# Kernel tuning notes

Measured on AMD Instinct MI355X. Metric: run time of the kernel, lower is better.

The kernel has to match this reference:

```python
import jax, jax.numpy as jnp
import numpy as np

B, NF, E, A = 4096, 40, 64, 32  # batch, num feature fields, embedding_size, attention_size


def setup_inputs() -> dict:
    key = jax.random.key(0)
    kx, kw, kb, kh = jax.random.split(key, 4)
    return {
        "x": jax.random.normal(kx, (B, NF, E), dtype=jnp.float32),
        "W": jax.random.normal(kw, (E, A), dtype=jnp.float32) * 0.05,  # random_normal init
        "b": jax.random.normal(kb, (A,), dtype=jnp.float32) * 0.05,
        "h": jax.random.normal(kh, (A,), dtype=jnp.float32) * 0.05,
        "p": jnp.ones((E, 1), dtype=jnp.float32),  # 'ones' initializer
    }


def reference(x, W, b, h, p):
    nf = x.shape[1]
    # pairwise (i<j) element-wise products, same ordering as the double loop
    ii, jj = np.triu_indices(nf, k=1)
    ewp = x[:, ii, :] * x[:, jj, :]                      # (B, P, E), P = nf*(nf-1)/2
    # attention MLP: relu(ewp @ W + b) . h, then exp-normalize over pairs
    a = jax.nn.relu(jnp.einsum('bpe,ea->bpa', ewp, W) + b)  # (B, P, A)
    e = jnp.exp(jnp.sum(a * h, axis=-1))                 # (B, P)  (faithful: no max-subtract)
    att = e / jnp.sum(e, axis=1, keepdims=True)          # (B, P)
    pooled = jnp.einsum('bp,bpe->be', att, ewp)          # attention-weighted sum over pairs
    return pooled @ p                                    # (B, 1)
```

## Files before the change

kernel.cpp:

```cpp
#include <hip/hip_runtime.h>

#define NFEAT 40
#define EMB   64
#define ATT   32
#define NPAIR 780
#define NTILE 49
#define XH_S  72
#define XREG  (NFEAT * XH_S)

#define WS_PRT   0
#define WS_WF    1024
#define WS_CONST 4096

typedef __attribute__((ext_vector_type(8))) _Float16 f16x8;
typedef __attribute__((ext_vector_type(4))) float    f32x4;
typedef __attribute__((ext_vector_type(2))) unsigned u32x2;

template <int CTRL>
__device__ __forceinline__ float dpp_add_f(float v) {
  int t = __builtin_amdgcn_update_dpp(0, __float_as_int(v), CTRL, 0xF, 0xF, true);
  return v + __int_as_float(t);
}
__device__ __forceinline__ float rowsum16(float v) {
  v = dpp_add_f<0x128>(v);
  v = dpp_add_f<0x124>(v);
  v = dpp_add_f<0x122>(v);
  v = dpp_add_f<0x121>(v);
  return v;
}
__device__ __forceinline__ float xgroup_sum(float v) {
#if __has_builtin(__builtin_amdgcn_permlane16_swap) && __has_builtin(__builtin_amdgcn_permlane32_swap)
  {
    auto a = __builtin_amdgcn_permlane16_swap(__float_as_uint(v), __float_as_uint(v), false, false);
    v = __uint_as_float(a[0]) + __uint_as_float(a[1]);
    auto b = __builtin_amdgcn_permlane32_swap(__float_as_uint(v), __float_as_uint(v), false, false);
    v = __uint_as_float(b[0]) + __uint_as_float(b[1]);
  }
#else
  v += __shfl_xor(v, 16, 64);
  v += __shfl_xor(v, 32, 64);
#endif
  return v;
}
__device__ __forceinline__ int pair_off(int i) { return 39 * i - (i * (i - 1)) / 2; }

extern "C" __global__ __launch_bounds__(256)
void afm_pre(const float* __restrict__ Wg, const float* __restrict__ bg,
             const float* __restrict__ hg, const float* __restrict__ pg,
             unsigned* __restrict__ ws) {
  __shared__ float Wl[EMB * ATT];
  const int tid = threadIdx.x;
  const float L2E = 1.4426950408889634f;

  if (blockIdx.x == 0) {
    for (int f = tid; f < EMB * ATT / 4; f += 256)
      *(float4*)&Wl[f * 4] = ((const float4*)Wg)[f];
    __syncthreads();
    for (int o = tid; o < 1536; o += 256) {
      int lane = o / 24, rem = o % 24, frag = rem >> 2, pi = rem & 3;
      int kk = frag / 3, which = frag % 3;
      int l15 = lane & 15, hk = lane >> 4;
      unsigned out = 0;
#pragma unroll
      for (int s = 0; s < 2; s++) {
        int t = pi * 2 + s;
        int krow = kk * 32 + hk * 8 + t;
        float v = (which == 0) ? Wl[krow * ATT + l15]
                : (which == 1) ? Wl[krow * ATT + 16 + l15]
                               : ((l15 == 0) ? pg[krow] : 0.f);
        _Float16 hv = (_Float16)v;
        unsigned short bits = __builtin_bit_cast(unsigned short, hv);
        out |= (unsigned)bits << (16 * s);
      }
      ws[WS_WF + lane * 24 + rem] = out;
    }
  } else if (blockIdx.x == 1) {
    for (int p = tid; p < NTILE * 16; p += 256) {
      int i = 0, j = 0;
      if (p < NPAIR) {
        i = (int)((79.0f - sqrtf(6241.0f - 8.0f * (float)p)) * 0.5f);
        if (i < 0) i = 0;
        while (pair_off(i + 1) <= p) ++i;
        while (pair_off(i) > p) --i;
        j = i + 1 + (p - pair_off(i));
      }
      int t = p >> 4, l = p & 15;
      ws[WS_PRT + (t >> 1) * 32 + l * 2 + (t & 1)] =
          (unsigned)(i * 144) | ((unsigned)(j * 144) << 16);
    }
  } else if (blockIdx.x == 2) {
    for (int o = tid; o < 1024; o += 256) {
      int lane = o >> 4, r = o & 15;
      int hk = lane >> 4, g = r >> 2, e = r & 3;
      float v;
      if (g == 0)      v = bg[hk * 4 + e];
      else if (g == 1) v = bg[16 + hk * 4 + e];
      else if (g == 2) v = hg[hk * 4 + e] * L2E;
      else             v = hg[16 + hk * 4 + e] * L2E;
      ((float*)ws)[WS_CONST + o] = v;
    }
  }
}

extern "C" __global__ __launch_bounds__(128)
void afm_kernel(const float* __restrict__ xg, const unsigned* __restrict__ ws,
                float* __restrict__ outg, int nbatch) {
  __shared__ __align__(16) _Float16 xh[2 * XREG];

  const int lane = threadIdx.x & 63, wid = threadIdx.x >> 6;
  const int l15 = lane & 15, hk = lane >> 4;
  const int bb = blockIdx.x * 2 + wid;
  if (bb >= nbatch) return;

  union { uint4 u; f16x8 h; } cv;
  const uint4* wfp = (const uint4*)(ws + WS_WF + lane * 24);
  f16x8 wf0[2], wf1[2], wf2[2];
  cv.u = wfp[0]; wf0[0] = cv.h;
  cv.u = wfp[1]; wf1[0] = cv.h;
  cv.u = wfp[2]; wf2[0] = cv.h;
  cv.u = wfp[3]; wf0[1] = cv.h;
  cv.u = wfp[4]; wf1[1] = cv.h;
  cv.u = wfp[5]; wf2[1] = cv.h;
  const float4* cp = (const float4*)((const float*)ws + WS_CONST + lane * 16);
  const float4 c0 = cp[0], c1 = cp[1];
  const float4 h0 = cp[2], h1 = cp[3];
  const f32x4 cb0 = {c0.x, c0.y, c0.z, c0.w};
  const f32x4 cb1 = {c1.x, c1.y, c1.z, c1.w};
  const f32x4 kz  = {0.f, 0.f, 0.f, 0.f};

  _Float16* xw = &xh[wid * XREG];
  const float* xsrc = xg + (size_t)bb * (NFEAT * EMB);
#pragma unroll
  for (int it = 0; it < 5; it++) {
    int g0 = (it * 64 + lane) * 8;
    float4 a = *(const float4*)&xsrc[g0];
    float4 b = *(const float4*)&xsrc[g0 + 4];
    int row = g0 >> 6, c = g0 & 63;
    f16x8 v = {(_Float16)a.x, (_Float16)a.y, (_Float16)a.z, (_Float16)a.w,
               (_Float16)b.x, (_Float16)b.y, (_Float16)b.z, (_Float16)b.w};
    *(f16x8*)&xw[row * XH_S + c] = v;
  }

  const unsigned wh = (unsigned)(wid * (XREG * 2) + hk * 16);
  float sum_e = 0.f, sum_es = 0.f;

  auto tile = [&](unsigned pij, bool full) {
    const unsigned offi = (pij & 0xFFFFu) + wh;
    const unsigned offj = (pij >> 16) + wh;
    const f16x8 xi0 = *(const f16x8*)((const char*)xh + offi);
    const f16x8 xj0 = *(const f16x8*)((const char*)xh + offj);
    const f16x8 xi1 = *(const f16x8*)((const char*)xh + offi + 64);
    const f16x8 xj1 = *(const f16x8*)((const char*)xh + offj + 64);
    f16x8 af0 = xi0 * xj0;
    f16x8 af1 = xi1 * xj1;
    f32x4 a0 = __builtin_amdgcn_mfma_f32_16x16x32_f16(wf0[0], af0, cb0, 0, 0, 0);
    f32x4 a1 = __builtin_amdgcn_mfma_f32_16x16x32_f16(wf1[0], af0, cb1, 0, 0, 0);
    f32x4 a2 = __builtin_amdgcn_mfma_f32_16x16x32_f16(wf2[0], af0, kz, 0, 0, 0);
    a0 = __builtin_amdgcn_mfma_f32_16x16x32_f16(wf0[1], af1, a0, 0, 0, 0);
    a1 = __builtin_amdgcn_mfma_f32_16x16x32_f16(wf1[1], af1, a1, 0, 0, 0);
    a2 = __builtin_amdgcn_mfma_f32_16x16x32_f16(wf2[1], af1, a2, 0, 0, 0);
    float t0 = fmaf(fmaxf(a0[0], 0.f), h0.x, fmaxf(a0[1], 0.f) * h0.y);
    float t1 = fmaf(fmaxf(a0[2], 0.f), h0.z, fmaxf(a0[3], 0.f) * h0.w);
    float t2 = fmaf(fmaxf(a1[0], 0.f), h1.x, fmaxf(a1[1], 0.f) * h1.y);
    float t3 = fmaf(fmaxf(a1[2], 0.f), h1.z, fmaxf(a1[3], 0.f) * h1.w);
    float v = xgroup_sum((t0 + t1) + (t2 + t3));
    float e = exp2f(v);
    if (!full) e = (l15 < 12) ? e : 0.f;
    sum_e += e;
    sum_es = fmaf(e, a2[0], sum_es);
  };

  u32x2 pp = *(const u32x2*)(ws + WS_PRT + l15 * 2);
#pragma unroll 4
  for (int k = 0; k < 24; ++k) {
    const unsigned pij0 = pp[0], pij1 = pp[1];
    if (k < 23) pp = *(const u32x2*)(ws + WS_PRT + (k + 1) * 32 + l15 * 2);
    tile(pij0, true);
    tile(pij1, true);
  }
  tile(ws[WS_PRT + 24 * 32 + l15 * 2], false);

  sum_e  = rowsum16(sum_e);
  sum_es = rowsum16(sum_es);
  if (lane == 0) outg[bb] = sum_es / sum_e;
}

extern "C" void kernel_launch(void* const* d_in, const int* in_sizes, int n_in,
                              void* d_out, int out_size, void* d_ws, size_t ws_size,
                              hipStream_t stream) {
  const float* xg = (const float*)d_in[0];
  const float* Wg = (const float*)d_in[1];
  const float* bg = (const float*)d_in[2];
  const float* hg = (const float*)d_in[3];
  const float* pg = (const float*)d_in[4];
  float* outg = (float*)d_out;
  unsigned* ws = (unsigned*)d_ws;
  const int Bn = in_sizes[0] / (NFEAT * EMB);
  afm_pre<<<dim3(3), dim3(256), 0, stream>>>(Wg, bg, hg, pg, ws);
  afm_kernel<<<dim3((Bn + 1) / 2), dim3(128), 0, stream>>>(xg, ws, outg, Bn);
}
```

Baseline: 41.38 us.

## Pack relu-dot epilogue into fp16 fdot2 and widen blocks to four waves

The attention epilogue now packs pairs of MFMA outputs to fp16, applies relu with a packed max and reduces against fp16-packed h using fdot2. This replaces eight scalar fmax/fma operations per tile. Blocks grow from two to four waves (one batch row each), the loop unroll rises to 8, and the x fp32→fp16 staging uses cvt_pkrtz. The change also adds a __syncthreads that is not needed, since each wave reads only its own shared-memory slice, and it lowers the precision of the h·relu dot.

New measurement: 41.61 us. No clear change (+0.6%).

```diff
diff --git a/kernel.cpp b/kernel.cpp
--- a/kernel.cpp
+++ b/kernel.cpp
@@ -15,6 +15,7 @@
 typedef __attribute__((ext_vector_type(8))) _Float16 f16x8;
 typedef __attribute__((ext_vector_type(4))) float    f32x4;
 typedef __attribute__((ext_vector_type(2))) unsigned u32x2;
+typedef __attribute__((ext_vector_type(2))) __fp16   h2_t;
 
 template <int CTRL>
 __device__ __forceinline__ float dpp_add_f(float v) {
@@ -43,6 +44,16 @@
   return v;
 }
 __device__ __forceinline__ int pair_off(int i) { return 39 * i - (i * (i - 1)) / 2; }
+
+__device__ __forceinline__ float reludot2(float s0, float s1, h2_t h2, float c) {
+  h2_t r = __builtin_amdgcn_cvt_pkrtz(s0, s1);
+  r = __builtin_elementwise_max(r, h2_t{(__fp16)0.f, (__fp16)0.f});
+#if __has_builtin(__builtin_amdgcn_fdot2)
+  return __builtin_amdgcn_fdot2(r, h2, c, false);
+#else
+  return fmaf((float)r[0], (float)h2[0], fmaf((float)r[1], (float)h2[1], c));
+#endif
+}
 
 extern "C" __global__ __launch_bounds__(256)
 void afm_pre(const float* __restrict__ Wg, const float* __restrict__ bg,
@@ -69,8 +80,7 @@
                 : (which == 1) ? Wl[krow * ATT + 16 + l15]
                                : ((l15 == 0) ? pg[krow] : 0.f);
         _Float16 hv = (_Float16)v;
-        unsigned short bits = __builtin_bit_cast(unsigned short, hv);
-        out |= (unsigned)bits << (16 * s);
+        out |= (unsigned)__builtin_bit_cast(unsigned short, hv) << (16 * s);
       }
       ws[WS_WF + lane * 24 + rem] = out;
     }
@@ -91,25 +101,31 @@
   } else if (blockIdx.x == 2) {
     for (int o = tid; o < 1024; o += 256) {
       int lane = o >> 4, r = o & 15;
-      int hk = lane >> 4, g = r >> 2, e = r & 3;
-      float v;
-      if (g == 0)      v = bg[hk * 4 + e];
-      else if (g == 1) v = bg[16 + hk * 4 + e];
-      else if (g == 2) v = hg[hk * 4 + e] * L2E;
-      else             v = hg[16 + hk * 4 + e] * L2E;
-      ((float*)ws)[WS_CONST + o] = v;
+      int hk = lane >> 4;
+      unsigned out;
+      if (r < 4) out = __float_as_uint(bg[hk * 4 + r]);
+      else if (r < 8) out = __float_as_uint(bg[16 + hk * 4 + (r - 4)]);
+      else if (r < 12) {
+        int q = r - 8;
+        int a0 = (q < 2) ? (hk * 4 + 2 * q) : (16 + hk * 4 + 2 * (q - 2));
+        __fp16 lo = (__fp16)(hg[a0] * L2E);
+        __fp16 hi = (__fp16)(hg[a0 + 1] * L2E);
+        out = (unsigned)__builtin_bit_cast(unsigned short, lo) |
+              ((unsigned)__builtin_bit_cast(unsigned short, hi) << 16);
+      } else out = 0;
+      ws[WS_CONST + o] = out;
     }
   }
 }
 
-extern "C" __global__ __launch_bounds__(128)
+extern "C" __global__ __launch_bounds__(256)
 void afm_kernel(const float* __restrict__ xg, const unsigned* __restrict__ ws,
                 float* __restrict__ outg, int nbatch) {
-  __shared__ __align__(16) _Float16 xh[2 * XREG];
+  __shared__ __align__(16) _Float16 xh[4 * XREG];
 
   const int lane = threadIdx.x & 63, wid = threadIdx.x >> 6;
   const int l15 = lane & 15, hk = lane >> 4;
-  const int bb = blockIdx.x * 2 + wid;
+  const int bb = blockIdx.x * 4 + wid;
   if (bb >= nbatch) return;
 
   union { uint4 u; f16x8 h; } cv;
@@ -121,12 +137,17 @@
   cv.u = wfp[3]; wf0[1] = cv.h;
   cv.u = wfp[4]; wf1[1] = cv.h;
   cv.u = wfp[5]; wf2[1] = cv.h;
-  const float4* cp = (const float4*)((const float*)ws + WS_CONST + lane * 16);
-  const float4 c0 = cp[0], c1 = cp[1];
-  const float4 h0 = cp[2], h1 = cp[3];
-  const f32x4 cb0 = {c0.x, c0.y, c0.z, c0.w};
-  const f32x4 cb1 = {c1.x, c1.y, c1.z, c1.w};
-  const f32x4 kz  = {0.f, 0.f, 0.f, 0.f};
+  const uint4* cp = (const uint4*)(ws + WS_CONST + lane * 16);
+  const uint4 u0 = cp[0], u1 = cp[1], u2 = cp[2];
+  const f32x4 cb0 = {__uint_as_float(u0.x), __uint_as_float(u0.y),
+                     __uint_as_float(u0.z), __uint_as_float(u0.w)};
+  const f32x4 cb1 = {__uint_as_float(u1.x), __uint_as_float(u1.y),
+                     __uint_as_float(u1.z), __uint_as_float(u1.w)};
+  union { unsigned u; h2_t h; } hcv;
+  hcv.u = u2.x; const h2_t hp0 = hcv.h;
+  hcv.u = u2.y; const h2_t hp1 = hcv.h;
+  hcv.u = u2.z; const h2_t hp2 = hcv.h;
+  hcv.u = u2.w; const h2_t hp3 = hcv.h;
 
   _Float16* xw = &xh[wid * XREG];
   const float* xsrc = xg + (size_t)bb * (NFEAT * EMB);
@@ -136,15 +157,20 @@
     float4 a = *(const float4*)&xsrc[g0];
     float4 b = *(const float4*)&xsrc[g0 + 4];
     int row = g0 >> 6, c = g0 & 63;
-    f16x8 v = {(_Float16)a.x, (_Float16)a.y, (_Float16)a.z, (_Float16)a.w,
-               (_Float16)b.x, (_Float16)b.y, (_Float16)b.z, (_Float16)b.w};
-    *(f16x8*)&xw[row * XH_S + c] = v;
-  }
+    union { h2_t v2[4]; f16x8 v8; } pk;
+    pk.v2[0] = __builtin_amdgcn_cvt_pkrtz(a.x, a.y);
+    pk.v2[1] = __builtin_amdgcn_cvt_pkrtz(a.z, a.w);
+    pk.v2[2] = __builtin_amdgcn_cvt_pkrtz(b.x, b.y);
+    pk.v2[3] = __builtin_amdgcn_cvt_pkrtz(b.z, b.w);
+    *(f16x8*)&xw[row * XH_S + c] = pk.v8;
+  }
+  __syncthreads();
 
   const unsigned wh = (unsigned)(wid * (XREG * 2) + hk * 16);
+  const f32x4 kz = {0.f, 0.f, 0.f, 0.f};
   float sum_e = 0.f, sum_es = 0.f;
 
-  auto tile = [&](unsigned pij, bool full) {
+  auto tile = [&](unsigned pij) {
     const unsigned offi = (pij & 0xFFFFu) + wh;
     const unsigned offj = (pij >> 16) + wh;
     const f16x8 xi0 = *(const f16x8*)((const char*)xh + offi);
@@ -159,26 +185,33 @@
     a0 = __builtin_amdgcn_mfma_f32_16x16x32_f16(wf0[1], af1, a0, 0, 0, 0);
     a1 = __builtin_amdgcn_mfma_f32_16x16x32_f16(wf1[1], af1, a1, 0, 0, 0);
     a2 = __builtin_amdgcn_mfma_f32_16x16x32_f16(wf2[1], af1, a2, 0, 0, 0);
-    float t0 = fmaf(fmaxf(a0[0], 0.f), h0.x, fmaxf(a0[1], 0.f) * h0.y);
-    float t1 = fmaf(fmaxf(a0[2], 0.f), h0.z, fmaxf(a0[3], 0.f) * h0.w);
-    float t2 = fmaf(fmaxf(a1[0], 0.f), h1.x, fmaxf(a1[1], 0.f) * h1.y);
-    float t3 = fmaf(fmaxf(a1[2], 0.f), h1.z, fmaxf(a1[3], 0.f) * h1.w);
-    float v = xgroup_sum((t0 + t1) + (t2 + t3));
+    float v = reludot2(a0[0], a0[1], hp0,
+              reludot2(a0[2], a0[3], hp1,
+              reludot2(a1[0], a1[1], hp2,
+              reludot2(a1[2], a1[3], hp3, 0.f))));
+    v = xgroup_sum(v);
     float e = exp2f(v);
-    if (!full) e = (l15 < 12) ? e : 0.f;
-    sum_e += e;
-    sum_es = fmaf(e, a2[0], sum_es);
+    return make_float2(e, a2[0]);
   };
 
   u32x2 pp = *(const u32x2*)(ws + WS_PRT + l15 * 2);
-#pragma unroll 4
+#pragma unroll 8
   for (int k = 0; k < 24; ++k) {
     const unsigned pij0 = pp[0], pij1 = pp[1];
     if (k < 23) pp = *(const u32x2*)(ws + WS_PRT + (k + 1) * 32 + l15 * 2);
-    tile(pij0, true);
-    tile(pij1, true);
-  }
-  tile(ws[WS_PRT + 24 * 32 + l15 * 2], false);
+    float2 rA = tile(pij0);
+    sum_e += rA.x;
+    sum_es = fmaf(rA.x, rA.y, sum_es);
+    float2 rB = tile(pij1);
+    sum_e += rB.x;
+    sum_es = fmaf(rB.x, rB.y, sum_es);
+  }
+  {
+    float2 rT = tile(ws[WS_PRT + 24 * 32 + l15 * 2]);
+    float e = (l15 < 12) ? rT.x : 0.f;
+    sum_e += e;
+    sum_es = fmaf(e, rT.y, sum_es);
+  }
 
   sum_e  = rowsum16(sum_e);
   sum_es = rowsum16(sum_es);
@@ -197,5 +230,5 @@
   unsigned* ws = (unsigned*)d_ws;
   const int Bn = in_sizes[0] / (NFEAT * EMB);
   afm_pre<<<dim3(3), dim3(256), 0, stream>>>(Wg, bg, hg, pg, ws);
-  afm_kernel<<<dim3((Bn + 1) / 2), dim3(128), 0, stream>>>(xg, ws, outg, Bn);
-}
+  afm_kernel<<<dim3((Bn + 3) / 4), dim3(256), 0, stream>>>(xg, ws, outg, Bn);
+}
```
